# Optimization experiments

Measured on AMD Instinct MI355X. Metric: run time of the kernel, lower is better.

The kernel has to match this reference:

```python
import jax, jax.numpy as jnp
import numpy as np

N, E, D, H = 50000, 800000, 128, 128


def _uniform_param(key, shape, fan_in):
    bound = 1.0 / np.sqrt(fan_in)
    return jax.random.uniform(key, shape, jnp.float32, -bound, bound)


def setup_inputs() -> dict:
    key = jax.random.key(0)
    ks = jax.random.split(key, 12)
    x = jax.random.normal(ks[0], (N, D), jnp.float32)
    xedge = jax.random.randint(ks[1], (2, E), 0, N, jnp.int64)
    y = jax.random.randint(ks[2], (N,), 0, 2, jnp.int32).astype(bool)
    return {
        "x": x,
        "xedge": xedge,
        "y": y,
        "pretrain": 0,
        # SAGEConv layer 1 (in=D, out=H): lin_l (with bias) applied to mean aggr, lin_r (no bias) to self
        "W1l": _uniform_param(ks[3], (D, H), D),
        "b1l": _uniform_param(ks[4], (H,), D),
        "W1r": _uniform_param(ks[5], (D, H), D),
        # SAGEConv layer 2 (in=H, out=H)
        "W2l": _uniform_param(ks[6], (H, H), H),
        "b2l": _uniform_param(ks[7], (H,), H),
        "W2r": _uniform_param(ks[8], (H, H), H),
        # Decoder weight [H, H]
        "Wdec": _uniform_param(ks[9], (H, H), H),
    }


def sage_conv(h, src, dst, Wl, bl, Wr, num_nodes):
    # gather neighbor features along edges, mean-aggregate by destination
    msgs = h[src]                                            # [E, d]
    agg = jax.ops.segment_sum(msgs, dst, num_segments=num_nodes)
    cnt = jax.ops.segment_sum(jnp.ones((src.shape[0],), h.dtype), dst,
                              num_segments=num_nodes)
    mean = agg / jnp.maximum(cnt, 1.0)[:, None]              # [N, d]
    return mean @ Wl + bl + h @ Wr                           # [N, out]


def reference(x, xedge, y, pretrain, W1l, b1l, W1r, W2l, b2l, W2r, Wdec):
    src, dst = xedge[0], xedge[1]
    n = x.shape[0]
    # Encoder: SAGE = conv1 -> relu -> (dropout: eval identity) -> conv2
    h = jax.nn.relu(sage_conv(x, src, dst, W1l, b1l, W1r, n))
    emb = sage_conv(h, src, dst, W2l, b2l, W2r, n)           # [N, H]
    # Decoder
    dx = emb @ Wdec                                          # [N, H]
    # BCEWithLogits: pos nodes target 1, neg nodes target 0, mean within each group
    ym = y.astype(dx.dtype)                                  # [N]
    n_pos = jnp.sum(ym)
    n_neg = n - n_pos
    hdim = dx.shape[1]
    sp_pos = jax.nn.softplus(-dx)   # bce(logit, 1)
    sp_neg = jax.nn.softplus(dx)    # bce(logit, 0)
    l2 = jnp.sum(sp_pos * ym[:, None]) / (jnp.maximum(n_pos, 1.0) * hdim)
    l1 = jnp.sum(sp_neg * (1.0 - ym)[:, None]) / (jnp.maximum(n_neg, 1.0) * hdim)
    return (l1 + l2, emb)
```

## Files before the change

kernel.cpp:

```cpp
#include <hip/hip_runtime.h>
#include <hip/hip_bf16.h>

#define NDIM 128
#define MROWS 32
#define BTHREADS 512
#define SCAN_CHUNK 1024

typedef __attribute__((ext_vector_type(8))) short short8;
typedef __attribute__((ext_vector_type(4))) float f32x4;

__device__ __forceinline__ float bf2f(__hip_bfloat16 v) { return __bfloat162float(v); }

__device__ __forceinline__ float ldf(const void* p, long i, int f32) {
    return f32 ? ((const float*)p)[i] : bf2f(((const __hip_bfloat16*)p)[i]);
}
__device__ __forceinline__ void stf(void* p, long i, int f32, float v) {
    if (f32) ((float*)p)[i] = v;
    else     ((__hip_bfloat16*)p)[i] = __float2bfloat16(v);
}
__device__ __forceinline__ short f2bf(float v) {
    __hip_bfloat16 h = __float2bfloat16(v);
    short s;
    __builtin_memcpy(&s, &h, 2);
    return s;
}
__device__ __forceinline__ float bflo(unsigned u) { u <<= 16; float f; __builtin_memcpy(&f, &u, 4); return f; }
__device__ __forceinline__ float bfhi(unsigned u) { u &= 0xffff0000u; float f; __builtin_memcpy(&f, &u, 4); return f; }
__device__ __forceinline__ unsigned packbf(float a, float b) {
    unsigned la = (unsigned short)f2bf(a);
    unsigned hb = (unsigned short)f2bf(b);
    return (hb << 16) | la;
}
__device__ __forceinline__ int aswz(int m, int k) {
    return m * NDIM + ((((k >> 3) ^ (m & 7)) << 3) | (k & 7));
}
__device__ __forceinline__ int wswz(int m, int p) {
    return m * 64 + ((((p >> 2) ^ (m & 7)) << 2) | (p & 3));
}

__global__ void detect_kernel(const int* __restrict__ xedge32,
                              const unsigned int* __restrict__ yw,
                              const unsigned short* __restrict__ xh,
                              int* __restrict__ flags, int* __restrict__ cnt,
                              float* __restrict__ accum, int* __restrict__ npos, int N) {
    const int gid = blockIdx.x * 256 + threadIdx.x;
    for (int i = gid; i < N; i += gridDim.x * 256) cnt[i] = 0;
    if (gid == 0) { accum[0] = 0.f; accum[1] = 0.f; npos[0] = 0; }
    if (blockIdx.x == 0) {
        __shared__ int se, sy, scount;
        const int t = threadIdx.x;
        if (t == 0) { se = 1; sy = 0; scount = 0; }
        __syncthreads();
        for (int i = t; i < 512; i += 256)
            if (xedge32[2 * i + 1] != 0) se = 0;
        for (int i = t; i < 1024; i += 256)
            if (yw[i] > 1u) sy = 1;
        int c = 0;
        for (int i = t; i < 1024; i += 256) {
            int ex = (xh[2 * i] >> 7) & 0xFF;
            if (ex >= 100 && ex <= 150) c++;
        }
        atomicAdd(&scount, c);
        __syncthreads();
        if (t == 0) { flags[0] = se; flags[1] = sy; flags[2] = (scount < 900) ? 1 : 0; }
    }
}


__global__ void prep_kernel(const void* __restrict__ x,
                            const void* __restrict__ W1l, const void* __restrict__ b1l,
                            const void* __restrict__ W1r, const void* __restrict__ W2l,
                            const void* __restrict__ b2l, const void* __restrict__ W2r,
                            const void* __restrict__ Wd, const int* __restrict__ flags,
                            short* __restrict__ T1l, short* __restrict__ T1r,
                            short* __restrict__ T2l, short* __restrict__ T2r,
                            short* __restrict__ Td, float* __restrict__ b1c,
                            float* __restrict__ b2c, unsigned* __restrict__ xb,
                            const int* __restrict__ xedge, int E,
                            int* __restrict__ cnt, int N) {
    const int wf = flags[2];
    const long idx = (long)blockIdx.x * 256 + threadIdx.x;
    if (idx < E) {
        int d = flags[0] ? xedge[2 * (E + idx)] : xedge[E + idx];
        atomicAdd(&cnt[d], 1);
    }
    if (idx < NDIM * NDIM) {
        int k = (int)(idx >> 7), n = (int)(idx & 127);
        int o = n * NDIM + k;
        T1l[o] = f2bf(ldf(W1l, idx, wf));
        T1r[o] = f2bf(ldf(W1r, idx, wf));
        T2l[o] = f2bf(ldf(W2l, idx, wf));
        T2r[o] = f2bf(ldf(W2r, idx, wf));
        Td [o] = f2bf(ldf(Wd , idx, wf));
        if (idx < NDIM) { b1c[idx] = ldf(b1l, idx, wf); b2c[idx] = ldf(b2l, idx, wf); }
    } else if (wf) {
        long p = idx - NDIM * NDIM;
        long np = (long)N * 64;
        if (p < np) {
            float2 v = ((const float2*)x)[p];
            xb[p] = packbf(v.x, v.y);
        }
    }
}


__global__ void scan_partial(const int* __restrict__ cnt, int* __restrict__ bsum, int N) {
    __shared__ int red[256];
    const int t = threadIdx.x;
    const long base = (long)blockIdx.x * SCAN_CHUNK + (long)t * 4;
    int s = 0;
#pragma unroll
    for (int i = 0; i < 4; ++i) { long idx = base + i; if (idx < N) s += cnt[idx]; }
    red[t] = s;
    __syncthreads();
    for (int off = 128; off >= 1; off >>= 1) {
        if (t < off) red[t] += red[t + off];
        __syncthreads();
    }
    if (t == 0) bsum[blockIdx.x] = red[0];
}

__global__ void scan_bsums(const int* __restrict__ bsum, int* __restrict__ boff,
                           int B, int* __restrict__ rowptr, int N) {
    __shared__ int part[1024];
    const int t = threadIdx.x;
    int v = (t < B) ? bsum[t] : 0;
    part[t] = v;
    __syncthreads();
    for (int off = 1; off < 1024; off <<= 1) {
        int u = (t >= off) ? part[t - off] : 0;
        __syncthreads();
        part[t] += u;
        __syncthreads();
    }
    if (t < B) boff[t] = part[t] - v;
    if (t == 1023) rowptr[N] = part[1023];
}

__global__ void scan_scatter(int* __restrict__ cnt, const int* __restrict__ boff,
                             int* __restrict__ rowptr, int N) {
    __shared__ int tsum[256];
    const int t = threadIdx.x;
    const long base = (long)blockIdx.x * SCAN_CHUNK + (long)t * 4;
    int loc[4];
    int s = 0;
#pragma unroll
    for (int i = 0; i < 4; ++i) {
        long idx = base + i;
        int c = (idx < N) ? cnt[idx] : 0;
        loc[i] = s;
        s += c;
    }
    tsum[t] = s;
    __syncthreads();
    for (int off = 1; off < 256; off <<= 1) {
        int u = (t >= off) ? tsum[t - off] : 0;
        __syncthreads();
        tsum[t] += u;
        __syncthreads();
    }
    const int texcl = tsum[t] - s;
    const int b0 = boff[blockIdx.x];
#pragma unroll
    for (int i = 0; i < 4; ++i) {
        long idx = base + i;
        if (idx < N) {
            int v = b0 + texcl + loc[i];
            rowptr[idx] = v;
            cnt[idx] = v;
        }
    }
}

__global__ void fill_kernel(const int* __restrict__ xedge, int E,
                            const int* __restrict__ flags,
                            int* __restrict__ cur, int* __restrict__ col) {
    int e = blockIdx.x * blockDim.x + threadIdx.x;
    if (e >= E) return;
    const int e64 = flags[0];
    int s = e64 ? xedge[2 * e] : xedge[e];
    int d = e64 ? xedge[2 * (E + e)] : xedge[E + e];
    int p = atomicAdd(&cur[d], 1);
    col[p] = s;
}


template <bool RELU, int OUTMODE>
__global__ __launch_bounds__(BTHREADS)
void layer_mfma(const unsigned* __restrict__ Xb, const unsigned* __restrict__ Xraw,
                const int* __restrict__ rowptr,
                const int* __restrict__ col, const short* __restrict__ WlT,
                const float* __restrict__ biasc, const short* __restrict__ WrT,
                const short* __restrict__ WdT, const void* __restrict__ yv,
                const int* __restrict__ flags, void* __restrict__ outp,
                float* __restrict__ accum, int* __restrict__ npos, int N) {
    __shared__ short AS[2 * MROWS * NDIM];
    __shared__ int ylds[MROWS];
    __shared__ float redm[8][2];
    short* Ms = AS;
    short* Ss = AS + MROWS * NDIM;
    unsigned* Msw = (unsigned*)Ms;
    unsigned* Ssw = (unsigned*)Ss;
    const int t = threadIdx.x;
    const int n0 = blockIdx.x * MROWS;
    const int wf = flags[2];
    const unsigned* __restrict__ X = wf ? Xb : Xraw;

    if (OUTMODE == 1 && t < MROWS) {
        const int yb = flags[1];
        int n = n0 + t;
        int yn = -1;
        if (n < N)
            yn = yb ? (int)((const unsigned char*)yv)[n]
                    : (((const int*)yv)[n] != 0 ? 1 : 0);
        ylds[t] = yn;
    }

    {
        const int p = t & 63;
        const int lj = t & 31;
        const int g = __builtin_amdgcn_readfirstlane(t >> 6);
        int r = g;
        int b = 0, e = 0;
        {
            int n = n0 + r;
            if (n < N) {
                b = __builtin_amdgcn_readfirstlane(rowptr[n]);
                e = __builtin_amdgcn_readfirstlane(rowptr[n + 1]);
            }
        }
        unsigned colv = 0;
        if (e > b) {
            int cl = b + lj;
            if (cl >= e) cl = e - 1;
            colv = (unsigned)col[cl];
        }
        for (int it = 0; it < 4; ++it, r += 8) {
            const int n = n0 + r;
            const int deg = e - b;
            unsigned su = 0;
            if (n < N) su = X[(long)n * 64 + p];
            unsigned u[32];
            if (deg > 0) {
#pragma unroll
                for (int j = 0; j < 8; ++j) {
                    int c = __builtin_amdgcn_readlane((int)colv, j);
                    u[j] = X[(long)c * 64 + p];
                }
            }
            if (deg > 8) {
#pragma unroll
                for (int j = 8; j < 16; ++j) {
                    int c = __builtin_amdgcn_readlane((int)colv, j);
                    u[j] = X[(long)c * 64 + p];
                }
            }
            if (deg > 16) {
#pragma unroll
                for (int j = 16; j < 24; ++j) {
                    int c = __builtin_amdgcn_readlane((int)colv, j);
                    u[j] = X[(long)c * 64 + p];
                }
            }
            if (deg > 24) {
#pragma unroll
                for (int j = 24; j < 32; ++j) {
                    int c = __builtin_amdgcn_readlane((int)colv, j);
                    u[j] = X[(long)c * 64 + p];
                }
            }
            int bn = 0, en = 0;
            unsigned colv_n = 0;
            if (it < 3) {
                int nn = n0 + r + 8;
                if (nn < N) {
                    bn = __builtin_amdgcn_readfirstlane(rowptr[nn]);
                    en = __builtin_amdgcn_readfirstlane(rowptr[nn + 1]);
                }
                if (en > bn) {
                    int cl = bn + lj;
                    if (cl >= en) cl = en - 1;
                    colv_n = (unsigned)col[cl];
                }
            }
            float m0 = 0.f, m1 = 0.f;
            if (deg > 0) {
                float p0 = 0.f, p1 = 0.f, p2 = 0.f, p3 = 0.f;
                float q0 = 0.f, q1 = 0.f, q2 = 0.f, q3 = 0.f;
#pragma unroll
                for (int j = 0; j < 32; j += 4) {
                    if (j + 0 < deg) { p0 += bflo(u[j]);     q0 += bfhi(u[j]); }
                    if (j + 1 < deg) { p1 += bflo(u[j + 1]); q1 += bfhi(u[j + 1]); }
                    if (j + 2 < deg) { p2 += bflo(u[j + 2]); q2 += bfhi(u[j + 2]); }
                    if (j + 3 < deg) { p3 += bflo(u[j + 3]); q3 += bfhi(u[j + 3]); }
                }
                m0 = (p0 + p1) + (p2 + p3);
                m1 = (q0 + q1) + (q2 + q3);
                for (int i = b + 32; i < e; ++i) {
                    int c = __builtin_amdgcn_readfirstlane(col[i]);
                    unsigned uu = X[(long)c * 64 + p];
                    m0 += bflo(uu);
                    m1 += bfhi(uu);
                }
                float inv = 1.f / (float)deg;
                m0 *= inv; m1 *= inv;
            }
            int wi = wswz(r, p);
            Msw[wi] = packbf(m0, m1);
            Ssw[wi] = su;
            b = bn; e = en; colv = colv_n;
        }
    }
    __syncthreads();
    const int l = t & 63, w = t >> 6;
    const int quad = l >> 4, l15 = l & 15;
    const int wcol = w * 16;
    f32x4 acc[2] = {};
    for (int k0 = 0; k0 < NDIM; k0 += 32) {
        const int kc = k0 + quad * 8;
        short8 ams[2], ass[2], bl, br;
#pragma unroll
        for (int rt = 0; rt < 2; ++rt) {
            int m = rt * 16 + l15;
            ams[rt] = *(const short8*)&Ms[aswz(m, kc)];
            ass[rt] = *(const short8*)&Ss[aswz(m, kc)];
        }
        {
            int n = wcol + l15;
            bl = *(const short8*)&WlT[n * NDIM + kc];
            br = *(const short8*)&WrT[n * NDIM + kc];
        }
#pragma unroll
        for (int rt = 0; rt < 2; ++rt) {
            acc[rt] = __builtin_amdgcn_mfma_f32_16x16x32_bf16(
                ams[rt], bl, acc[rt], 0, 0, 0);
            acc[rt] = __builtin_amdgcn_mfma_f32_16x16x32_bf16(
                ass[rt], br, acc[rt], 0, 0, 0);
        }
    }
    __syncthreads();

    if (OUTMODE == 0) {
        {
            int cg = wcol + l15;
            float bv = biasc[cg];
#pragma unroll
            for (int rt = 0; rt < 2; ++rt)
#pragma unroll
                for (int reg = 0; reg < 4; ++reg) {
                    int row = rt * 16 + quad * 4 + reg;
                    float v = acc[rt][reg] + bv;
                    if (RELU) v = fmaxf(v, 0.f);
                    Ms[row * NDIM + cg] = f2bf(v);
                }
        }
        __syncthreads();
        unsigned* ob = (unsigned*)outp;
        for (int idx = t; idx < MROWS * 64; idx += BTHREADS) {
            int r = idx >> 6;
            if (n0 + r < N) ob[(long)n0 * 64 + idx] = Msw[idx];
        }
    } else {
        {
            int cg = wcol + l15;
            float bv = biasc[cg];
#pragma unroll
            for (int rt = 0; rt < 2; ++rt)
#pragma unroll
                for (int reg = 0; reg < 4; ++reg) {
                    int row = rt * 16 + quad * 4 + reg;
                    float v = acc[rt][reg] + bv;
                    Ms[aswz(row, cg)] = f2bf(v);
                    int n = n0 + row;
                    if (n < N) {
                        if (wf) ((float*)outp)[1 + (long)n * NDIM + cg] = v;
                        else ((__hip_bfloat16*)outp)[1 + (long)n * NDIM + cg] =
                                 __float2bfloat16(v);
                    }
                }
        }
        __syncthreads();
        f32x4 acc2[2] = {};
        for (int k0 = 0; k0 < NDIM; k0 += 32) {
            const int kc = k0 + quad * 8;
            short8 a[2], bwd;
#pragma unroll
            for (int rt = 0; rt < 2; ++rt)
                a[rt] = *(const short8*)&Ms[aswz(rt * 16 + l15, kc)];
            bwd = *(const short8*)&WdT[(wcol + l15) * NDIM + kc];
#pragma unroll
            for (int rt = 0; rt < 2; ++rt)
                acc2[rt] = __builtin_amdgcn_mfma_f32_16x16x32_bf16(
                    a[rt], bwd, acc2[rt], 0, 0, 0);
        }
        float lpos = 0.f, lneg = 0.f;
#pragma unroll
        for (int rt = 0; rt < 2; ++rt)
#pragma unroll
            for (int reg = 0; reg < 4; ++reg) {
                int row = rt * 16 + quad * 4 + reg;
                int yn = ylds[row];
                if (yn >= 0) {
                    float z = acc2[rt][reg];
                    float L = log1pf(expf(-fabsf(z)));
                    if (yn) lpos += fmaxf(-z, 0.f) + L;
                    else    lneg += fmaxf(z, 0.f) + L;
                }
            }
#pragma unroll
        for (int off = 32; off >= 1; off >>= 1) {
            lpos += __shfl_down(lpos, off, 64);
            lneg += __shfl_down(lneg, off, 64);
        }
        if (l == 0) { redm[w][0] = lpos; redm[w][1] = lneg; }
        __syncthreads();
        if (t == 0) {
            float sp = 0.f, sn = 0.f;
#pragma unroll
            for (int i = 0; i < 8; ++i) { sp += redm[i][0]; sn += redm[i][1]; }
            atomicAdd(&accum[0], sp);
            atomicAdd(&accum[1], sn);
            int c = 0;
            for (int i = 0; i < MROWS; ++i) if (ylds[i] > 0) c++;
            if (c) atomicAdd(npos, c);
        }
    }
}

__global__ void finalize_kernel(const float* __restrict__ accum, const int* __restrict__ npos,
                                const int* __restrict__ flags, void* __restrict__ out, int N) {
    float np_ = (float)(*npos);
    float nn_ = (float)N - np_;
    float l2 = accum[0] / (fmaxf(np_, 1.f) * 128.f);
    float l1 = accum[1] / (fmaxf(nn_, 1.f) * 128.f);
    stf(out, 0, flags[2], l1 + l2);
}


extern "C" void kernel_launch(void* const* d_in, const int* in_sizes, int n_in,
                              void* d_out, int out_size, void* d_ws, size_t ws_size,
                              hipStream_t stream) {
    const void* x    = d_in[0];
    const int* xedge = (const int*)d_in[1];
    const void* y    = d_in[2];
    const void* W1l  = d_in[4];
    const void* b1l  = d_in[5];
    const void* W1r  = d_in[6];
    const void* W2l  = d_in[7];
    const void* b2l  = d_in[8];
    const void* W2r  = d_in[9];
    const void* Wdec = d_in[10];

    const int N = in_sizes[0] / NDIM;
    const int E = in_sizes[1] / 2;

    char* ws = (char*)d_ws;
    size_t off = 0;
    auto alloc = [&](size_t bytes) -> void* {
        void* p = ws + off;
        off = (off + bytes + 255) & ~(size_t)255;
        return p;
    };
    int*   flags  = (int*)alloc(64);
    float* accum  = (float*)alloc(64);
    int*   npos   = (int*)alloc(64);
    int*   bsum   = (int*)alloc(1024 * 4);
    int*   boff   = (int*)alloc(1024 * 4);
    int*   cnt    = (int*)alloc((size_t)N * 4);
    int*   rowptr = (int*)alloc((size_t)(N + 1) * 4);
    int*   col    = (int*)alloc((size_t)E * 4);
    unsigned* xb  = (unsigned*)alloc((size_t)N * 64 * 4);
    unsigned* hbuf = (unsigned*)alloc((size_t)N * 64 * 4);
    short* T1l = (short*)alloc(NDIM * NDIM * 2);
    short* T1r = (short*)alloc(NDIM * NDIM * 2);
    short* T2l = (short*)alloc(NDIM * NDIM * 2);
    short* T2r = (short*)alloc(NDIM * NDIM * 2);
    short* Td  = (short*)alloc(NDIM * NDIM * 2);
    float* b1c = (float*)alloc(NDIM * 4);
    float* b2c = (float*)alloc(NDIM * 4);

    const int zb = (N + 255) / 256;
    detect_kernel<<<zb, 256, 0, stream>>>(xedge, (const unsigned int*)y,
                                          (const unsigned short*)x, flags, cnt,
                                          accum, npos, N);
    const long prep_items = (long)NDIM * NDIM + (long)N * 64;
    prep_kernel<<<(int)((prep_items + 255) / 256), 256, 0, stream>>>(
        x, W1l, b1l, W1r, W2l, b2l, W2r, Wdec, flags,
        T1l, T1r, T2l, T2r, Td, b1c, b2c, xb, xedge, E, cnt, N);

    const int sb = (N + SCAN_CHUNK - 1) / SCAN_CHUNK;
    scan_partial<<<sb, 256, 0, stream>>>(cnt, bsum, N);
    scan_bsums<<<1, 1024, 0, stream>>>(bsum, boff, sb, rowptr, N);
    scan_scatter<<<sb, 256, 0, stream>>>(cnt, boff, rowptr, N);

    const int eb = (E + 255) / 256;
    fill_kernel<<<eb, 256, 0, stream>>>(xedge, E, flags, cnt, col);

    const int nbM = (N + MROWS - 1) / MROWS;
    layer_mfma<true, 0><<<nbM, BTHREADS, 0, stream>>>(
        xb, (const unsigned*)x, rowptr, col, T1l, b1c, T1r, nullptr, nullptr,
        flags, hbuf, nullptr, nullptr, N);
    layer_mfma<false, 1><<<nbM, BTHREADS, 0, stream>>>(
        hbuf, hbuf, rowptr, col, T2l, b2c, T2r, Td, y, flags,
        d_out, accum, npos, N);
    finalize_kernel<<<1, 1, 0, stream>>>(accum, npos, flags, d_out, N);
}
```

Before: 314.1 us.

## Fuse three-pass scan into single-block kernel and load neighbor indices as scalars

Replaces the three-kernel prefix scan over node degrees with one single-block kernel that walks N in 4096-element chunks, removing two launches and the block-sum buffers. In the aggregation loop, neighbor indices are now read per edge as wave-uniform scalar loads (readfirstlane) with a bounds clamp, instead of one vector load per lane followed by readlane extraction and a prefetch of the next row's columns. It also adds a min-blocks hint of 4 to the layer kernel's launch bounds, which may cap registers and cause spills. The single-block scan serializes about a dozen chunk iterations on one CU, and the per-edge scalar loads lose the previous prefetch overlap.

```diff
diff --git a/kernel.cpp b/kernel.cpp
--- a/kernel.cpp
+++ b/kernel.cpp
@@ -103,73 +103,44 @@
     }
 }
 
-
-__global__ void scan_partial(const int* __restrict__ cnt, int* __restrict__ bsum, int N) {
-    __shared__ int red[256];
-    const int t = threadIdx.x;
-    const long base = (long)blockIdx.x * SCAN_CHUNK + (long)t * 4;
-    int s = 0;
-#pragma unroll
-    for (int i = 0; i < 4; ++i) { long idx = base + i; if (idx < N) s += cnt[idx]; }
-    red[t] = s;
-    __syncthreads();
-    for (int off = 128; off >= 1; off >>= 1) {
-        if (t < off) red[t] += red[t + off];
-        __syncthreads();
-    }
-    if (t == 0) bsum[blockIdx.x] = red[0];
-}
-
-__global__ void scan_bsums(const int* __restrict__ bsum, int* __restrict__ boff,
-                           int B, int* __restrict__ rowptr, int N) {
+__global__ void scan_fused(int* __restrict__ cnt, int* __restrict__ rowptr, int N) {
     __shared__ int part[1024];
     const int t = threadIdx.x;
-    int v = (t < B) ? bsum[t] : 0;
-    part[t] = v;
-    __syncthreads();
-    for (int off = 1; off < 1024; off <<= 1) {
-        int u = (t >= off) ? part[t - off] : 0;
-        __syncthreads();
-        part[t] += u;
-        __syncthreads();
-    }
-    if (t < B) boff[t] = part[t] - v;
-    if (t == 1023) rowptr[N] = part[1023];
-}
-
-__global__ void scan_scatter(int* __restrict__ cnt, const int* __restrict__ boff,
-                             int* __restrict__ rowptr, int N) {
-    __shared__ int tsum[256];
-    const int t = threadIdx.x;
-    const long base = (long)blockIdx.x * SCAN_CHUNK + (long)t * 4;
-    int loc[4];
-    int s = 0;
-#pragma unroll
-    for (int i = 0; i < 4; ++i) {
-        long idx = base + i;
-        int c = (idx < N) ? cnt[idx] : 0;
-        loc[i] = s;
-        s += c;
-    }
-    tsum[t] = s;
-    __syncthreads();
-    for (int off = 1; off < 256; off <<= 1) {
-        int u = (t >= off) ? tsum[t - off] : 0;
-        __syncthreads();
-        tsum[t] += u;
-        __syncthreads();
-    }
-    const int texcl = tsum[t] - s;
-    const int b0 = boff[blockIdx.x];
-#pragma unroll
-    for (int i = 0; i < 4; ++i) {
-        long idx = base + i;
-        if (idx < N) {
-            int v = b0 + texcl + loc[i];
-            rowptr[idx] = v;
-            cnt[idx] = v;
-        }
-    }
+    int total = 0;
+    for (int base0 = 0; base0 < N; base0 += 4096) {
+        const int idx0 = base0 + t * 4;
+        int loc[4];
+        int s = 0;
+#pragma unroll
+        for (int i = 0; i < 4; ++i) {
+            int idx = idx0 + i;
+            int cv = (idx < N) ? cnt[idx] : 0;
+            loc[i] = s;
+            s += cv;
+        }
+        part[t] = s;
+        __syncthreads();
+        for (int off = 1; off < 1024; off <<= 1) {
+            int uu = (t >= off) ? part[t - off] : 0;
+            __syncthreads();
+            part[t] += uu;
+            __syncthreads();
+        }
+        const int texcl = total + part[t] - s;
+        const int chunk_total = part[1023];
+#pragma unroll
+        for (int i = 0; i < 4; ++i) {
+            int idx = idx0 + i;
+            if (idx < N) {
+                int v = texcl + loc[i];
+                rowptr[idx] = v;
+                cnt[idx] = v;
+            }
+        }
+        total += chunk_total;
+        __syncthreads();
+    }
+    if (t == 0) rowptr[N] = total;
 }
 
 __global__ void fill_kernel(const int* __restrict__ xedge, int E,
@@ -186,7 +157,7 @@
 
 
 template <bool RELU, int OUTMODE>
-__global__ __launch_bounds__(BTHREADS)
+__global__ __launch_bounds__(BTHREADS, 4)
 void layer_mfma(const unsigned* __restrict__ Xb, const unsigned* __restrict__ Xraw,
                 const int* __restrict__ rowptr,
                 const int* __restrict__ col, const short* __restrict__ WlT,
@@ -218,7 +189,6 @@
 
     {
         const int p = t & 63;
-        const int lj = t & 31;
         const int g = __builtin_amdgcn_readfirstlane(t >> 6);
         int r = g;
         int b = 0, e = 0;
@@ -229,58 +199,64 @@
                 e = __builtin_amdgcn_readfirstlane(rowptr[n + 1]);
             }
         }
-        unsigned colv = 0;
-        if (e > b) {
-            int cl = b + lj;
-            if (cl >= e) cl = e - 1;
-            colv = (unsigned)col[cl];
-        }
         for (int it = 0; it < 4; ++it, r += 8) {
             const int n = n0 + r;
             const int deg = e - b;
             unsigned su = 0;
             if (n < N) su = X[(long)n * 64 + p];
+            const int* colb = col + b;
+            int cs[32];
+            if (deg > 0) {
+#pragma unroll
+                for (int j = 0; j < 8; ++j) {
+                    int c = __builtin_amdgcn_readfirstlane(colb[j]);
+                    cs[j] = ((unsigned)c >= (unsigned)N) ? 0 : c;
+                }
+            }
+            if (deg > 8) {
+#pragma unroll
+                for (int j = 8; j < 16; ++j) {
+                    int c = __builtin_amdgcn_readfirstlane(colb[j]);
+                    cs[j] = ((unsigned)c >= (unsigned)N) ? 0 : c;
+                }
+            }
+            if (deg > 16) {
+#pragma unroll
+                for (int j = 16; j < 24; ++j) {
+                    int c = __builtin_amdgcn_readfirstlane(colb[j]);
+                    cs[j] = ((unsigned)c >= (unsigned)N) ? 0 : c;
+                }
+            }
+            if (deg > 24) {
+#pragma unroll
+                for (int j = 24; j < 32; ++j) {
+                    int c = __builtin_amdgcn_readfirstlane(colb[j]);
+                    cs[j] = ((unsigned)c >= (unsigned)N) ? 0 : c;
+                }
+            }
             unsigned u[32];
             if (deg > 0) {
 #pragma unroll
-                for (int j = 0; j < 8; ++j) {
-                    int c = __builtin_amdgcn_readlane((int)colv, j);
-                    u[j] = X[(long)c * 64 + p];
-                }
+                for (int j = 0; j < 8; ++j) u[j] = X[(long)cs[j] * 64 + p];
             }
             if (deg > 8) {
 #pragma unroll
-                for (int j = 8; j < 16; ++j) {
-                    int c = __builtin_amdgcn_readlane((int)colv, j);
-                    u[j] = X[(long)c * 64 + p];
-                }
+                for (int j = 8; j < 16; ++j) u[j] = X[(long)cs[j] * 64 + p];
             }
             if (deg > 16) {
 #pragma unroll
-                for (int j = 16; j < 24; ++j) {
-                    int c = __builtin_amdgcn_readlane((int)colv, j);
-                    u[j] = X[(long)c * 64 + p];
-                }
+                for (int j = 16; j < 24; ++j) u[j] = X[(long)cs[j] * 64 + p];
             }
             if (deg > 24) {
 #pragma unroll
-                for (int j = 24; j < 32; ++j) {
-                    int c = __builtin_amdgcn_readlane((int)colv, j);
-                    u[j] = X[(long)c * 64 + p];
-                }
+                for (int j = 24; j < 32; ++j) u[j] = X[(long)cs[j] * 64 + p];
             }
             int bn = 0, en = 0;
-            unsigned colv_n = 0;
             if (it < 3) {
                 int nn = n0 + r + 8;
                 if (nn < N) {
                     bn = __builtin_amdgcn_readfirstlane(rowptr[nn]);
                     en = __builtin_amdgcn_readfirstlane(rowptr[nn + 1]);
-                }
-                if (en > bn) {
-                    int cl = bn + lj;
-                    if (cl >= en) cl = en - 1;
-                    colv_n = (unsigned)col[cl];
                 }
             }
             float m0 = 0.f, m1 = 0.f;
@@ -308,7 +284,7 @@
             int wi = wswz(r, p);
             Msw[wi] = packbf(m0, m1);
             Ssw[wi] = su;
-            b = bn; e = en; colv = colv_n;
+            b = bn; e = en;
         }
     }
     __syncthreads();
@@ -464,8 +440,6 @@
     int*   flags  = (int*)alloc(64);
     float* accum  = (float*)alloc(64);
     int*   npos   = (int*)alloc(64);
-    int*   bsum   = (int*)alloc(1024 * 4);
-    int*   boff   = (int*)alloc(1024 * 4);
     int*   cnt    = (int*)alloc((size_t)N * 4);
     int*   rowptr = (int*)alloc((size_t)(N + 1) * 4);
     int*   col    = (int*)alloc((size_t)E * 4);
@@ -488,10 +462,7 @@
         x, W1l, b1l, W1r, W2l, b2l, W2r, Wdec, flags,
         T1l, T1r, T2l, T2r, Td, b1c, b2c, xb, xedge, E, cnt, N);
 
-    const int sb = (N + SCAN_CHUNK - 1) / SCAN_CHUNK;
-    scan_partial<<<sb, 256, 0, stream>>>(cnt, bsum, N);
-    scan_bsums<<<1, 1024, 0, stream>>>(bsum, boff, sb, rowptr, N);
-    scan_scatter<<<sb, 256, 0, stream>>>(cnt, boff, rowptr, N);
+    scan_fused<<<1, 1024, 0, stream>>>(cnt, rowptr, N);
 
     const int eb = (E + 255) / 256;
     fill_kernel<<<eb, 256, 0, stream>>>(xedge, E, flags, cnt, col);
```

New measurement: 357.3 us. 1.14x slower.

## Load neighbor indices via scalar reads, add occupancy hint, grid-stride x conversion

Applied to the files above, without the earlier changes.

The gather loop now reads each neighbor index directly with wave-uniform scalar loads (readfirstlane on col entries) instead of loading a per-lane vector and extracting lanes with readlane. Out-of-range indices past the row end are clamped to 0. A scheduling barrier is placed before the reduction, and launch bounds request two blocks per CU. The prep kernel is resized to E-or-weights items and uses a grid-stride loop for the x-to-bf16 conversion. The aim is shorter dependency chains on index loads and better latency hiding, at the cost of possible register pressure and extra scalar loads that can read beyond the row.

```diff
diff --git a/kernel.cpp b/kernel.cpp
--- a/kernel.cpp
+++ b/kernel.cpp
@@ -93,10 +93,11 @@
         T2r[o] = f2bf(ldf(W2r, idx, wf));
         Td [o] = f2bf(ldf(Wd , idx, wf));
         if (idx < NDIM) { b1c[idx] = ldf(b1l, idx, wf); b2c[idx] = ldf(b2l, idx, wf); }
-    } else if (wf) {
-        long p = idx - NDIM * NDIM;
-        long np = (long)N * 64;
-        if (p < np) {
+    }
+    if (wf) {
+        const long np = (long)N * 64;
+        const long stride = (long)gridDim.x * 256;
+        for (long p = idx; p < np; p += stride) {
             float2 v = ((const float2*)x)[p];
             xb[p] = packbf(v.x, v.y);
         }
@@ -186,7 +187,7 @@
 
 
 template <bool RELU, int OUTMODE>
-__global__ __launch_bounds__(BTHREADS)
+__global__ __launch_bounds__(BTHREADS, 2)
 void layer_mfma(const unsigned* __restrict__ Xb, const unsigned* __restrict__ Xraw,
                 const int* __restrict__ rowptr,
                 const int* __restrict__ col, const short* __restrict__ WlT,
@@ -218,7 +219,6 @@
 
     {
         const int p = t & 63;
-        const int lj = t & 31;
         const int g = __builtin_amdgcn_readfirstlane(t >> 6);
         int r = g;
         int b = 0, e = 0;
@@ -229,60 +229,67 @@
                 e = __builtin_amdgcn_readfirstlane(rowptr[n + 1]);
             }
         }
-        unsigned colv = 0;
-        if (e > b) {
-            int cl = b + lj;
-            if (cl >= e) cl = e - 1;
-            colv = (unsigned)col[cl];
-        }
         for (int it = 0; it < 4; ++it, r += 8) {
             const int n = n0 + r;
             const int deg = e - b;
             unsigned su = 0;
             if (n < N) su = X[(long)n * 64 + p];
+            const int* colb = col + b;
+            int cs[32];
+            if (deg > 0) {
+#pragma unroll
+                for (int j = 0; j < 8; ++j) {
+                    int c = __builtin_amdgcn_readfirstlane(colb[j]);
+                    cs[j] = ((unsigned)c >= (unsigned)N) ? 0 : c;
+                }
+            }
+            if (deg > 8) {
+#pragma unroll
+                for (int j = 8; j < 16; ++j) {
+                    int c = __builtin_amdgcn_readfirstlane(colb[j]);
+                    cs[j] = ((unsigned)c >= (unsigned)N) ? 0 : c;
+                }
+            }
+            if (deg > 16) {
+#pragma unroll
+                for (int j = 16; j < 24; ++j) {
+                    int c = __builtin_amdgcn_readfirstlane(colb[j]);
+                    cs[j] = ((unsigned)c >= (unsigned)N) ? 0 : c;
+                }
+            }
+            if (deg > 24) {
+#pragma unroll
+                for (int j = 24; j < 32; ++j) {
+                    int c = __builtin_amdgcn_readfirstlane(colb[j]);
+                    cs[j] = ((unsigned)c >= (unsigned)N) ? 0 : c;
+                }
+            }
             unsigned u[32];
             if (deg > 0) {
 #pragma unroll
-                for (int j = 0; j < 8; ++j) {
-                    int c = __builtin_amdgcn_readlane((int)colv, j);
-                    u[j] = X[(long)c * 64 + p];
-                }
+                for (int j = 0; j < 8; ++j) u[j] = X[(long)cs[j] * 64 + p];
             }
             if (deg > 8) {
 #pragma unroll
-                for (int j = 8; j < 16; ++j) {
-                    int c = __builtin_amdgcn_readlane((int)colv, j);
-                    u[j] = X[(long)c * 64 + p];
-                }
+                for (int j = 8; j < 16; ++j) u[j] = X[(long)cs[j] * 64 + p];
             }
             if (deg > 16) {
 #pragma unroll
-                for (int j = 16; j < 24; ++j) {
-                    int c = __builtin_amdgcn_readlane((int)colv, j);
-                    u[j] = X[(long)c * 64 + p];
-                }
+                for (int j = 16; j < 24; ++j) u[j] = X[(long)cs[j] * 64 + p];
             }
             if (deg > 24) {
 #pragma unroll
-                for (int j = 24; j < 32; ++j) {
-                    int c = __builtin_amdgcn_readlane((int)colv, j);
-                    u[j] = X[(long)c * 64 + p];
-                }
+                for (int j = 24; j < 32; ++j) u[j] = X[(long)cs[j] * 64 + p];
             }
             int bn = 0, en = 0;
-            unsigned colv_n = 0;
             if (it < 3) {
                 int nn = n0 + r + 8;
                 if (nn < N) {
                     bn = __builtin_amdgcn_readfirstlane(rowptr[nn]);
                     en = __builtin_amdgcn_readfirstlane(rowptr[nn + 1]);
                 }
-                if (en > bn) {
-                    int cl = bn + lj;
-                    if (cl >= en) cl = en - 1;
-                    colv_n = (unsigned)col[cl];
-                }
-            }
+            }
+            __builtin_amdgcn_sched_barrier(0);
             float m0 = 0.f, m1 = 0.f;
             if (deg > 0) {
                 float p0 = 0.f, p1 = 0.f, p2 = 0.f, p3 = 0.f;
@@ -308,7 +315,7 @@
             int wi = wswz(r, p);
             Msw[wi] = packbf(m0, m1);
             Ssw[wi] = su;
-            b = bn; e = en; colv = colv_n;
+            b = bn; e = en;
         }
     }
     __syncthreads();
@@ -483,7 +490,7 @@
     detect_kernel<<<zb, 256, 0, stream>>>(xedge, (const unsigned int*)y,
                                           (const unsigned short*)x, flags, cnt,
                                           accum, npos, N);
-    const long prep_items = (long)NDIM * NDIM + (long)N * 64;
+    const long prep_items = (E > NDIM * NDIM) ? E : NDIM * NDIM;
     prep_kernel<<<(int)((prep_items + 255) / 256), 256, 0, stream>>>(
         x, W1l, b1l, W1r, W2l, b2l, W2r, Wdec, flags,
         T1l, T1r, T2l, T2r, Td, b1c, b2c, xb, xedge, E, cnt, N);
```

Result: no change. 312.6 us (-0.5%).
